# Performance work log

Measured on AMD Instinct MI355X. Metric: run time of the kernel, lower is better.

The kernel has to match this reference:

```python
import jax, jax.numpy as jnp
import numpy as np

SIGMA = 2.0
Z_CUTOFF = 3


def make_gaussian_kernel(sigma=SIGMA, z=Z_CUTOFF):
    # kernel_size = 2*z*sigma + 1; bump to odd if even (float math as in torch)
    ks = 2 * z * sigma + 1
    if ks % 2 == 0:
        ks += 1
    ks = int(ks)
    r = np.arange(-(ks // 2), ks // 2 + 1, dtype=np.float32)
    xx, yy = np.meshgrid(r, r, indexing='ij')
    k = np.exp(-(xx ** 2 + yy ** 2) / (2.0 * sigma ** 2))
    k = k / k.sum()
    return jnp.asarray(k.reshape(1, 1, ks, ks))  # [O=1, I=1, kh, kw]


def setup_inputs() -> dict:
    key = jax.random.key(0)
    x = jax.random.normal(key, (32, 1, 1024, 1024), dtype=jnp.float32)
    kernel = make_gaussian_kernel()
    return {"x": x, "kernel": kernel}


def reference(x, kernel):
    ks = kernel.shape[-1]
    half = ks // 2
    h_even_in = x.shape[-2] % 2 == 0
    w_even_in = x.shape[-1] % 2 == 0
    # torch F.pad order (left, right, top, bottom) -> jnp.pad ((top,bot),(left,right))
    pad_t, pad_b = half, half + int(h_even_in)
    pad_l, pad_r = half, half + int(w_even_in)
    xp = jnp.pad(x, ((0, 0), (0, 0), (pad_t, pad_b), (pad_l, pad_r)), mode='reflect')
    # cross-correlation, valid padding (matches torch conv2d with padding=0)
    y = jax.lax.conv_general_dilated(
        xp, kernel, window_strides=(1, 1), padding='VALID',
        dimension_numbers=('NCHW', 'OIHW', 'NCHW'))
    # crop based on parity of POST-conv shape, as in the torch module
    h_cut = 2 if y.shape[-2] % 2 == 0 else 1
    w_cut = 2 if y.shape[-1] % 2 == 0 else 1
    return y[:, :, :-h_cut, :-w_cut]
```

## Files before the change

### kernel.cpp

```cpp
#include <hip/hip_runtime.h>

#define KS    13
#define HALF  6
#define TY    32
#define NITER (TY + 12)
#define NK    (NITER / 2)
#define IMG_H 1024
#define IMG_W 1024

__device__ __forceinline__ int reflect_idx(int i, int n) {
    if (i < 0) i = -i;
    if (i >= n) i = 2 * n - 2 - i;
    return i;
}

struct Ctx {
    const float* xin;
    float*       o;
    float        g[KS];
    int          t;
    int          r0;
    bool         interior;
};

__device__ __forceinline__ float4 h_filter(const float* srow, const Ctx& cx) {
    float f[20];
    if (cx.interior) {
        #pragma unroll
        for (int k = 0; k < 5; ++k) {
            float4 v = *reinterpret_cast<const float4*>(srow + 4 * cx.t - 8 + 4 * k);
            f[4*k+0] = v.x; f[4*k+1] = v.y; f[4*k+2] = v.z; f[4*k+3] = v.w;
        }
    } else {
        #pragma unroll
        for (int k = 0; k < 20; ++k)
            f[k] = srow[reflect_idx(4 * cx.t - 8 + k, IMG_W)];
    }
    float4 h = make_float4(0.f, 0.f, 0.f, 0.f);
    #pragma unroll
    for (int j = 0; j < KS; ++j) {
        h.x += cx.g[j] * f[2 + j];
        h.y += cx.g[j] * f[3 + j];
        h.z += cx.g[j] * f[4 + j];
        h.w += cx.g[j] * f[5 + j];
    }
    return h;
}

template<int U>
__device__ __forceinline__ void body2(int outer, const Ctx& cx, float (*s)[IMG_W],
                                      float4 (&w)[14], float4& cur0, float4& cur1)
{
    const int k = outer * 7 + U;
    if (k >= NK) return;
    const int n0 = 2 * k;
    const int bp = (k & 1) * 2;

    *reinterpret_cast<float4*>(&s[bp + 0][4 * cx.t]) = cur0;
    *reinterpret_cast<float4*>(&s[bp + 1][4 * cx.t]) = cur1;
    if (k + 1 < NK) {
        const int ra = reflect_idx(cx.r0 + n0 - 4, IMG_H);
        const int rb = reflect_idx(cx.r0 + n0 - 3, IMG_H);
        cur0 = *reinterpret_cast<const float4*>(cx.xin + (size_t)ra * IMG_W + 4 * cx.t);
        cur1 = *reinterpret_cast<const float4*>(cx.xin + (size_t)rb * IMG_W + 4 * cx.t);
    }
    __syncthreads();

    w[(2 * U) % 14]     = h_filter(s[bp + 0], cx);
    w[(2 * U + 1) % 14] = h_filter(s[bp + 1], cx);

    if (n0 >= 12) {
        float4 a0 = make_float4(0.f, 0.f, 0.f, 0.f);
        float4 a1 = make_float4(0.f, 0.f, 0.f, 0.f);
        #pragma unroll
        for (int j = 0; j < KS; ++j) {
            const float4 v0 = w[(2 * U + 2 + j) % 14];
            const float4 v1 = w[(2 * U + 3 + j) % 14];
            a0.x += cx.g[j] * v0.x;  a1.x += cx.g[j] * v1.x;
            a0.y += cx.g[j] * v0.y;  a1.y += cx.g[j] * v1.y;
            a0.z += cx.g[j] * v0.z;  a1.z += cx.g[j] * v1.z;
            a0.w += cx.g[j] * v0.w;  a1.w += cx.g[j] * v1.w;
        }
        *reinterpret_cast<float4*>(cx.o + (size_t)(cx.r0 + n0 - 12) * IMG_W + 4 * cx.t) = a0;
        *reinterpret_cast<float4*>(cx.o + (size_t)(cx.r0 + n0 - 11) * IMG_W + 4 * cx.t) = a1;
    }
}

__global__ __launch_bounds__(256) void gauss_blur_stream(
    const float* __restrict__ x, const float* __restrict__ k2d,
    float* __restrict__ out)
{
    __shared__ float s[4][IMG_W];

    Ctx cx;
    cx.t  = threadIdx.x;
    cx.r0 = blockIdx.x * TY;
    const int img = blockIdx.y;
    cx.xin = x + (size_t)img * IMG_H * IMG_W;
    cx.o   = out + (size_t)img * IMG_H * IMG_W;
    cx.interior = (cx.t >= 2) && (cx.t <= 253);

    {
        float c   = k2d[HALF * KS + HALF];
        float inv = 1.0f / sqrtf(c);
        #pragma unroll
        for (int j = 0; j < KS; ++j) cx.g[j] = k2d[j * KS + HALF] * inv;
    }

    float4 w[14];
    float4 cur0 = *reinterpret_cast<const float4*>(
        cx.xin + (size_t)reflect_idx(cx.r0 - 6, IMG_H) * IMG_W + 4 * cx.t);
    float4 cur1 = *reinterpret_cast<const float4*>(
        cx.xin + (size_t)reflect_idx(cx.r0 - 5, IMG_H) * IMG_W + 4 * cx.t);

    for (int outer = 0; outer < 4; ++outer) {
        body2<0>(outer, cx, s, w, cur0, cur1);
        body2<1>(outer, cx, s, w, cur0, cur1);
        body2<2>(outer, cx, s, w, cur0, cur1);
        body2<3>(outer, cx, s, w, cur0, cur1);
        body2<4>(outer, cx, s, w, cur0, cur1);
        body2<5>(outer, cx, s, w, cur0, cur1);
        body2<6>(outer, cx, s, w, cur0, cur1);
    }
}

extern "C" void kernel_launch(void* const* d_in, const int* in_sizes, int n_in,
                              void* d_out, int out_size, void* d_ws, size_t ws_size,
                              hipStream_t stream) {
    const float* x   = (const float*)d_in[0];
    const float* k2d = (const float*)d_in[1];
    float*       out = (float*)d_out;

    dim3 grid(IMG_H / TY, 32);
    gauss_blur_stream<<<grid, 256, 0, stream>>>(x, k2d, out);
}
```

Measured before the change: 54.45 us.

## Split image width into 256-column segments with single-wavefront blocks and halos

Each block now covers a 256-column segment of 32 rows using one 64-thread wavefront, with an 8-column halo on each side staged in a small shared buffer. The grid gains a width dimension, so it has four times as many blocks, and the per-block shared memory shrinks from 16 KB to about 4 KB. Because a single-wave block is used, the __syncthreads barriers become cheap and occupancy can rise. In exchange, halo columns are re-read from global memory by neighbouring segments, a few lanes do extra loads, and edge granules take a per-element reflect path.

```diff
diff --git a/kernel.cpp b/kernel.cpp
--- a/kernel.cpp
+++ b/kernel.cpp
@@ -3,6 +3,8 @@
 #define KS    13
 #define HALF  6
 #define TY    32
+#define SEG   256
+#define SW    272
 #define NITER (TY + 12)
 #define NK    (NITER / 2)
 #define IMG_H 1024
@@ -18,23 +20,28 @@
     const float* xin;
     float*       o;
     float        g[KS];
-    int          t;
+    int          lane;
+    int          c0;
     int          r0;
-    bool         interior;
 };
+
+__device__ __forceinline__ float4 load_gran(const float* rowp, int gc0) {
+    if (gc0 >= 0 && gc0 <= IMG_W - 4)
+        return *reinterpret_cast<const float4*>(rowp + gc0);
+    float4 v;
+    v.x = rowp[reflect_idx(gc0 + 0, IMG_W)];
+    v.y = rowp[reflect_idx(gc0 + 1, IMG_W)];
+    v.z = rowp[reflect_idx(gc0 + 2, IMG_W)];
+    v.w = rowp[reflect_idx(gc0 + 3, IMG_W)];
+    return v;
+}
 
 __device__ __forceinline__ float4 h_filter(const float* srow, const Ctx& cx) {
     float f[20];
-    if (cx.interior) {
-        #pragma unroll
-        for (int k = 0; k < 5; ++k) {
-            float4 v = *reinterpret_cast<const float4*>(srow + 4 * cx.t - 8 + 4 * k);
-            f[4*k+0] = v.x; f[4*k+1] = v.y; f[4*k+2] = v.z; f[4*k+3] = v.w;
-        }
-    } else {
-        #pragma unroll
-        for (int k = 0; k < 20; ++k)
-            f[k] = srow[reflect_idx(4 * cx.t - 8 + k, IMG_W)];
+    #pragma unroll
+    for (int k = 0; k < 5; ++k) {
+        float4 v = *reinterpret_cast<const float4*>(srow + 4 * cx.lane + 4 * k);
+        f[4*k+0] = v.x; f[4*k+1] = v.y; f[4*k+2] = v.z; f[4*k+3] = v.w;
     }
     float4 h = make_float4(0.f, 0.f, 0.f, 0.f);
     #pragma unroll
@@ -48,21 +55,35 @@
 }
 
 template<int U>
-__device__ __forceinline__ void body2(int outer, const Ctx& cx, float (*s)[IMG_W],
-                                      float4 (&w)[14], float4& cur0, float4& cur1)
+__device__ __forceinline__ void body2(int outer, const Ctx& cx, float (*s)[SW],
+                                      float4 (&w)[14],
+                                      float4& cA0, float4& cB0,
+                                      float4& cA1, float4& cB1)
 {
     const int k = outer * 7 + U;
     if (k >= NK) return;
     const int n0 = 2 * k;
     const int bp = (k & 1) * 2;
+    const bool hasB = cx.lane < 4;
 
-    *reinterpret_cast<float4*>(&s[bp + 0][4 * cx.t]) = cur0;
-    *reinterpret_cast<float4*>(&s[bp + 1][4 * cx.t]) = cur1;
+    *reinterpret_cast<float4*>(&s[bp + 0][4 * cx.lane]) = cA0;
+    *reinterpret_cast<float4*>(&s[bp + 1][4 * cx.lane]) = cA1;
+    if (hasB) {
+        *reinterpret_cast<float4*>(&s[bp + 0][256 + 4 * cx.lane]) = cB0;
+        *reinterpret_cast<float4*>(&s[bp + 1][256 + 4 * cx.lane]) = cB1;
+    }
+
     if (k + 1 < NK) {
-        const int ra = reflect_idx(cx.r0 + n0 - 4, IMG_H);
-        const int rb = reflect_idx(cx.r0 + n0 - 3, IMG_H);
-        cur0 = *reinterpret_cast<const float4*>(cx.xin + (size_t)ra * IMG_W + 4 * cx.t);
-        cur1 = *reinterpret_cast<const float4*>(cx.xin + (size_t)rb * IMG_W + 4 * cx.t);
+        const float* ra = cx.xin + (size_t)reflect_idx(cx.r0 + n0 - 4, IMG_H) * IMG_W;
+        const float* rb = cx.xin + (size_t)reflect_idx(cx.r0 + n0 - 3, IMG_H) * IMG_W;
+        const int gA = cx.c0 - 8 + 4 * cx.lane;
+        cA0 = load_gran(ra, gA);
+        cA1 = load_gran(rb, gA);
+        if (hasB) {
+            const int gB = cx.c0 - 8 + 4 * (64 + cx.lane);
+            cB0 = load_gran(ra, gB);
+            cB1 = load_gran(rb, gB);
+        }
     }
     __syncthreads();
 
@@ -81,24 +102,26 @@
             a0.z += cx.g[j] * v0.z;  a1.z += cx.g[j] * v1.z;
             a0.w += cx.g[j] * v0.w;  a1.w += cx.g[j] * v1.w;
         }
-        *reinterpret_cast<float4*>(cx.o + (size_t)(cx.r0 + n0 - 12) * IMG_W + 4 * cx.t) = a0;
-        *reinterpret_cast<float4*>(cx.o + (size_t)(cx.r0 + n0 - 11) * IMG_W + 4 * cx.t) = a1;
+        float* d0 = cx.o + (size_t)(cx.r0 + n0 - 12) * IMG_W + cx.c0 + 4 * cx.lane;
+        float* d1 = cx.o + (size_t)(cx.r0 + n0 - 11) * IMG_W + cx.c0 + 4 * cx.lane;
+        *reinterpret_cast<float4*>(d0) = a0;
+        *reinterpret_cast<float4*>(d1) = a1;
     }
 }
 
-__global__ __launch_bounds__(256) void gauss_blur_stream(
+__global__ __launch_bounds__(64) void gauss_blur_stream(
     const float* __restrict__ x, const float* __restrict__ k2d,
     float* __restrict__ out)
 {
-    __shared__ float s[4][IMG_W];
+    __shared__ float s[4][SW];
 
     Ctx cx;
-    cx.t  = threadIdx.x;
-    cx.r0 = blockIdx.x * TY;
-    const int img = blockIdx.y;
+    cx.lane = threadIdx.x;
+    cx.c0   = blockIdx.x * SEG;
+    cx.r0   = blockIdx.y * TY;
+    const int img = blockIdx.z;
     cx.xin = x + (size_t)img * IMG_H * IMG_W;
     cx.o   = out + (size_t)img * IMG_H * IMG_W;
-    cx.interior = (cx.t >= 2) && (cx.t <= 253);
 
     {
         float c   = k2d[HALF * KS + HALF];
@@ -107,20 +130,25 @@
         for (int j = 0; j < KS; ++j) cx.g[j] = k2d[j * KS + HALF] * inv;
     }
 
+    const bool hasB = cx.lane < 4;
+    const int  gA   = cx.c0 - 8 + 4 * cx.lane;
+    const int  gB   = cx.c0 - 8 + 4 * (64 + cx.lane);
+    const float* ra = cx.xin + (size_t)reflect_idx(cx.r0 - 6, IMG_H) * IMG_W;
+    const float* rb = cx.xin + (size_t)reflect_idx(cx.r0 - 5, IMG_H) * IMG_W;
+    float4 cA0 = load_gran(ra, gA);
+    float4 cA1 = load_gran(rb, gA);
+    float4 cB0 = hasB ? load_gran(ra, gB) : make_float4(0,0,0,0);
+    float4 cB1 = hasB ? load_gran(rb, gB) : make_float4(0,0,0,0);
+
     float4 w[14];
-    float4 cur0 = *reinterpret_cast<const float4*>(
-        cx.xin + (size_t)reflect_idx(cx.r0 - 6, IMG_H) * IMG_W + 4 * cx.t);
-    float4 cur1 = *reinterpret_cast<const float4*>(
-        cx.xin + (size_t)reflect_idx(cx.r0 - 5, IMG_H) * IMG_W + 4 * cx.t);
-
     for (int outer = 0; outer < 4; ++outer) {
-        body2<0>(outer, cx, s, w, cur0, cur1);
-        body2<1>(outer, cx, s, w, cur0, cur1);
-        body2<2>(outer, cx, s, w, cur0, cur1);
-        body2<3>(outer, cx, s, w, cur0, cur1);
-        body2<4>(outer, cx, s, w, cur0, cur1);
-        body2<5>(outer, cx, s, w, cur0, cur1);
-        body2<6>(outer, cx, s, w, cur0, cur1);
+        body2<0>(outer, cx, s, w, cA0, cB0, cA1, cB1);
+        body2<1>(outer, cx, s, w, cA0, cB0, cA1, cB1);
+        body2<2>(outer, cx, s, w, cA0, cB0, cA1, cB1);
+        body2<3>(outer, cx, s, w, cA0, cB0, cA1, cB1);
+        body2<4>(outer, cx, s, w, cA0, cB0, cA1, cB1);
+        body2<5>(outer, cx, s, w, cA0, cB0, cA1, cB1);
+        body2<6>(outer, cx, s, w, cA0, cB0, cA1, cB1);
     }
 }
 
@@ -131,6 +159,6 @@
     const float* k2d = (const float*)d_in[1];
     float*       out = (float*)d_out;
 
-    dim3 grid(IMG_H / TY, 32);
-    gauss_blur_stream<<<grid, 256, 0, stream>>>(x, k2d, out);
+    dim3 grid(IMG_W / SEG, IMG_H / TY, 32);
+    gauss_blur_stream<<<grid, 64, 0, stream>>>(x, k2d, out);
 }
```

Measured after the change: 72.91 us. 1.34x slower.

## Stage input rows via direct global-to-LDS loads and use nontemporal output stores

Applied to the files above, without the earlier changes.

Replaces the register-staged row prefetch (global load into registers, then store into shared memory) with async global_load_lds builtins that write 16-byte chunks straight into the double-buffered LDS rows. The barrier moves to the end of each step so the next pair of rows loads while the current pair is filtered. Output writes become nontemporal stores to reduce cache pollution. The change depends on the wave-base LDS addressing and on barrier ordering being enough to wait for the async loads, which could introduce races if the vmcnt wait is not emitted.

```diff
diff --git a/kernel.cpp b/kernel.cpp
--- a/kernel.cpp
+++ b/kernel.cpp
@@ -7,6 +7,11 @@
 #define NK    (NITER / 2)
 #define IMG_H 1024
 #define IMG_W 1024
+
+#define GLOBAL_AS __attribute__((address_space(1)))
+#define LDS_AS    __attribute__((address_space(3)))
+
+typedef float vfloat4 __attribute__((ext_vector_type(4)));
 
 __device__ __forceinline__ int reflect_idx(int i, int n) {
     if (i < 0) i = -i;
@@ -22,6 +27,18 @@
     int          r0;
     bool         interior;
 };
+
+__device__ __forceinline__ void stage2(const Ctx& cx, float (*s)[IMG_W], int k) {
+    const int bp = (k & 1) * 2;
+    const int ra = reflect_idx(cx.r0 + 2 * k - 6, IMG_H);
+    const int rb = reflect_idx(cx.r0 + 2 * k - 5, IMG_H);
+    const float* pa = cx.xin + (size_t)ra * IMG_W + 4 * cx.t;
+    const float* pb = cx.xin + (size_t)rb * IMG_W + 4 * cx.t;
+    float* la = &s[bp + 0][4 * (cx.t & ~63)];
+    float* lb = &s[bp + 1][4 * (cx.t & ~63)];
+    __builtin_amdgcn_global_load_lds((const GLOBAL_AS void*)pa, (LDS_AS void*)la, 16, 0, 0);
+    __builtin_amdgcn_global_load_lds((const GLOBAL_AS void*)pb, (LDS_AS void*)lb, 16, 0, 0);
+}
 
 __device__ __forceinline__ float4 h_filter(const float* srow, const Ctx& cx) {
     float f[20];
@@ -47,24 +64,21 @@
     return h;
 }
 
+__device__ __forceinline__ void nt_store4(float* p, const float4& a) {
+    vfloat4 v = { a.x, a.y, a.z, a.w };
+    __builtin_nontemporal_store(v, reinterpret_cast<vfloat4*>(p));
+}
+
 template<int U>
 __device__ __forceinline__ void body2(int outer, const Ctx& cx, float (*s)[IMG_W],
-                                      float4 (&w)[14], float4& cur0, float4& cur1)
+                                      float4 (&w)[14])
 {
     const int k = outer * 7 + U;
     if (k >= NK) return;
     const int n0 = 2 * k;
     const int bp = (k & 1) * 2;
 
-    *reinterpret_cast<float4*>(&s[bp + 0][4 * cx.t]) = cur0;
-    *reinterpret_cast<float4*>(&s[bp + 1][4 * cx.t]) = cur1;
-    if (k + 1 < NK) {
-        const int ra = reflect_idx(cx.r0 + n0 - 4, IMG_H);
-        const int rb = reflect_idx(cx.r0 + n0 - 3, IMG_H);
-        cur0 = *reinterpret_cast<const float4*>(cx.xin + (size_t)ra * IMG_W + 4 * cx.t);
-        cur1 = *reinterpret_cast<const float4*>(cx.xin + (size_t)rb * IMG_W + 4 * cx.t);
-    }
-    __syncthreads();
+    if (k + 1 < NK) stage2(cx, s, k + 1);
 
     w[(2 * U) % 14]     = h_filter(s[bp + 0], cx);
     w[(2 * U + 1) % 14] = h_filter(s[bp + 1], cx);
@@ -81,9 +95,11 @@
             a0.z += cx.g[j] * v0.z;  a1.z += cx.g[j] * v1.z;
             a0.w += cx.g[j] * v0.w;  a1.w += cx.g[j] * v1.w;
         }
-        *reinterpret_cast<float4*>(cx.o + (size_t)(cx.r0 + n0 - 12) * IMG_W + 4 * cx.t) = a0;
-        *reinterpret_cast<float4*>(cx.o + (size_t)(cx.r0 + n0 - 11) * IMG_W + 4 * cx.t) = a1;
+        nt_store4(cx.o + (size_t)(cx.r0 + n0 - 12) * IMG_W + 4 * cx.t, a0);
+        nt_store4(cx.o + (size_t)(cx.r0 + n0 - 11) * IMG_W + 4 * cx.t, a1);
     }
+
+    if (k + 1 < NK) __syncthreads();
 }
 
 __global__ __launch_bounds__(256) void gauss_blur_stream(
@@ -107,20 +123,18 @@
         for (int j = 0; j < KS; ++j) cx.g[j] = k2d[j * KS + HALF] * inv;
     }
 
+    stage2(cx, s, 0);
+    __syncthreads();
+
     float4 w[14];
-    float4 cur0 = *reinterpret_cast<const float4*>(
-        cx.xin + (size_t)reflect_idx(cx.r0 - 6, IMG_H) * IMG_W + 4 * cx.t);
-    float4 cur1 = *reinterpret_cast<const float4*>(
-        cx.xin + (size_t)reflect_idx(cx.r0 - 5, IMG_H) * IMG_W + 4 * cx.t);
-
     for (int outer = 0; outer < 4; ++outer) {
-        body2<0>(outer, cx, s, w, cur0, cur1);
-        body2<1>(outer, cx, s, w, cur0, cur1);
-        body2<2>(outer, cx, s, w, cur0, cur1);
-        body2<3>(outer, cx, s, w, cur0, cur1);
-        body2<4>(outer, cx, s, w, cur0, cur1);
-        body2<5>(outer, cx, s, w, cur0, cur1);
-        body2<6>(outer, cx, s, w, cur0, cur1);
+        body2<0>(outer, cx, s, w);
+        body2<1>(outer, cx, s, w);
+        body2<2>(outer, cx, s, w);
+        body2<3>(outer, cx, s, w);
+        body2<4>(outer, cx, s, w);
+        body2<5>(outer, cx, s, w);
+        body2<6>(outer, cx, s, w);
     }
 }
 
```

After: 58.45 us. 1.07x slower.
